# Optimization experiments

Hardware: AMD Instinct MI355X
Metric: run time of the kernel (lower is better)

The kernel has to match this reference:

```python
import jax, jax.numpy as jnp
import numpy as np

LATENT = 128
K = 1024          # num_embeddings
LENGTH = 128
HID = 200         # LSTM hidden
IN = 768
COND = 1536


def setup_inputs() -> dict:
    key = jax.random.key(0)
    ks = jax.random.split(key, 16)
    B = 256
    x = jax.random.normal(ks[0], (B, 1, LENGTH, IN), dtype=jnp.float32)
    condition = jax.random.normal(ks[1], (B, 1, LENGTH, COND), dtype=jnp.float32)
    noise = jax.random.normal(ks[2], (B, IN), dtype=jnp.float32)
    s = 0.05
    # LSTM params (PyTorch gate order: i, f, g, o)
    W_ih = jax.random.normal(ks[3], (4 * HID, IN), dtype=jnp.float32) * s
    W_hh = jax.random.normal(ks[4], (4 * HID, HID), dtype=jnp.float32) * s
    b_ih = jax.random.normal(ks[5], (4 * HID,), dtype=jnp.float32) * s
    b_hh = jax.random.normal(ks[6], (4 * HID,), dtype=jnp.float32) * s
    # encoder fc: HID -> LATENT
    W_enc = jax.random.normal(ks[7], (LATENT, HID), dtype=jnp.float32) * s
    b_enc = jnp.zeros((LATENT,), dtype=jnp.float32)
    # codebook, uniform(-1/K, 1/K) as in the module
    emb = jax.random.uniform(ks[8], (K, LATENT), minval=-1.0 / K, maxval=1.0 / K, dtype=jnp.float32)
    # decoder MLP
    D1_IN = LATENT + COND + IN  # 2432
    W1 = jax.random.normal(ks[9], (200, D1_IN), dtype=jnp.float32) * s
    b1 = jnp.zeros((200,), dtype=jnp.float32)
    W2 = jax.random.normal(ks[10], (400, 200), dtype=jnp.float32) * s
    b2 = jnp.zeros((400,), dtype=jnp.float32)
    W3 = jax.random.normal(ks[11], (IN, 400), dtype=jnp.float32) * s
    b3 = jnp.zeros((IN,), dtype=jnp.float32)
    return {"x": x, "condition": condition, "noise": noise,
            "W_ih": W_ih, "W_hh": W_hh, "b_ih": b_ih, "b_hh": b_hh,
            "W_enc": W_enc, "b_enc": b_enc, "emb": emb,
            "W1": W1, "b1": b1, "W2": W2, "b2": b2, "W3": W3, "b3": b3}


def _lstm_last_h(xs, W_ih, W_hh, b_ih, b_hh):
    # xs: [B, T, IN] -> final hidden state [B, HID]
    B = xs.shape[0]
    h0 = jnp.zeros((B, HID), dtype=xs.dtype)
    c0 = jnp.zeros((B, HID), dtype=xs.dtype)
    # precompute input projections for all timesteps: [T, B, 4H]
    gates_x = jnp.einsum('bti,gi->tbg', xs, W_ih) + b_ih + b_hh

    def step(carry, gx):
        h, c = carry
        g = gx + h @ W_hh.T  # [B, 4H]
        i, f, gg, o = jnp.split(g, 4, axis=-1)
        c = jax.nn.sigmoid(f) * c + jax.nn.sigmoid(i) * jnp.tanh(gg)
        h = jax.nn.sigmoid(o) * jnp.tanh(c)
        return (h, c), None

    (h, _), _ = jax.lax.scan(step, (h0, c0), gates_x)
    return h


def reference(x, condition, noise, W_ih, W_hh, b_ih, b_hh, W_enc, b_enc, emb,
              W1, b1, W2, b2, W3, b3):
    B = x.shape[0]
    # Encoder
    xs = x.reshape(B, -1, IN)                      # [B, T, 768]
    h = _lstm_last_h(xs, W_ih, W_hh, b_ih, b_hh)   # [B, 200]
    z_e = h @ W_enc.T + b_enc                      # [B, latent]
    # VectorQuantizer: squared-distance argmin + gather
    d = (jnp.sum(z_e * z_e, axis=-1, keepdims=True)
         + jnp.sum(emb * emb, axis=1)
         - 2.0 * z_e @ emb.T)                      # [B, K]
    indices = jnp.argmin(d, axis=-1)               # [B]
    z_q = emb[indices]                             # [B, latent]
    # Decoder (forward uses z_q directly)
    L = LENGTH
    z = jnp.broadcast_to(z_q[:, None, None, :], (B, 1, L, LATENT))
    n = jnp.broadcast_to(noise[:, None, None, :], (B, 1, L, IN))
    zc = jnp.concatenate([z, condition, n], axis=-1)  # [B,1,L,2432]
    h1 = jax.nn.relu(zc @ W1.T + b1)
    h2 = jax.nn.relu(h1 @ W2.T + b2)
    out = jax.nn.sigmoid(h2 @ W3.T + b3)
    return out.reshape(-1, 1, L, IN)
```

## Files before the change

### kernel.cpp

```cpp
#include <hip/hip_runtime.h>
#include <math.h>

typedef unsigned short u16;
typedef u16 u16x8 __attribute__((ext_vector_type(8)));
typedef __bf16 bf16x8 __attribute__((ext_vector_type(8)));
typedef float f32x4 __attribute__((ext_vector_type(4)));

#define HID 200
#define G4H 800
#define TLEN 128
#define LATENT 128
#define NCODES 1024
#define DIN 768
#define DCOND 1536
#define NB 256
#define MROWS (NB * TLEN)
#define LDG 896
#define LDH1 256
#define LDH2 512
#define NOUT 768

#define WSCL 400.0f
#define HSCL 127.0f
#define ISCL (1.0f / (WSCL * HSCL))
#define W4_UINT4 (12 * 800)
#define W4_BYTES (W4_UINT4 * 16)

__device__ __forceinline__ u16 f2b(float f) {
  union { float f; unsigned u; } v; v.f = f;
  unsigned r = v.u + 0x7fffu + ((v.u >> 16) & 1u);
  return (u16)(r >> 16);
}
__device__ __forceinline__ float b2f(u16 h) {
  union { unsigned u; float f; } v; v.u = ((unsigned)h) << 16;
  return v.f;
}
__device__ __forceinline__ float sigf(float x) { return 1.f / (1.f + __expf(-x)); }
__device__ __forceinline__ float tanh_fast(float x) {
  return 1.f - 2.f / (__expf(2.f * x) + 1.f);
}

__device__ __forceinline__ int dot4(unsigned a, unsigned b, int c) {
#if __has_builtin(__builtin_amdgcn_sdot4)
  return __builtin_amdgcn_sdot4((int)a, (int)b, c, false);
#else
  int s = c;
  s += (int)(signed char)(a) * (int)(signed char)(b);
  s += (int)(signed char)(a >> 8) * (int)(signed char)(b >> 8);
  s += (int)(signed char)(a >> 16) * (int)(signed char)(b >> 16);
  s += (int)(signed char)(a >> 24) * (int)(signed char)(b >> 24);
  return s;
#endif
}

__device__ __forceinline__ void gl16(const void* g, void* l) {
  __builtin_amdgcn_global_load_lds(
      (const __attribute__((address_space(1))) void*)g,
      (__attribute__((address_space(3))) void*)l, 16, 0, 0);
}

__device__ __forceinline__ unsigned cvtpk(float a, float b) {
  unsigned r;
  asm("v_cvt_pk_bf16_f32 %0, %1, %2" : "=v"(r) : "v"(a), "v"(b));
  return r;
}

__global__ void cvt_pad(const float* __restrict__ src, u16* __restrict__ dst,
                        int nr, int nc, int lds, int col0, int NRp, int KP) {
  int i = blockIdx.x * blockDim.x + threadIdx.x;
  if (i >= NRp * KP) return;
  int r = i / KP, c = i - r * KP;
  float v = (r < nr && c < nc) ? src[(size_t)r * lds + col0 + c] : 0.f;
  dst[i] = f2b(v);
}

__global__ void pad_f32(const float* __restrict__ src, float* __restrict__ dst,
                        int n, int npad) {
  int i = blockIdx.x * blockDim.x + threadIdx.x;
  if (i < npad) dst[i] = (i < n) ? src[i] : 0.f;
}

__global__ void pack_whh_i8(const float* __restrict__ Whh, unsigned* __restrict__ W4,
                            unsigned* __restrict__ Wreg,
                            const float* __restrict__ b_ih, const float* __restrict__ b_hh,
                            float* __restrict__ biasc) {
  int i = blockIdx.x * blockDim.x + threadIdx.x;
  if (i < 800 * 50) {
    int row = i / 50, dw = i - row * 50;
    unsigned d = 0;
#pragma unroll
    for (int e = 0; e < 4; ++e) {
      int k = dw * 4 + e;
      float w = Whh[(size_t)row * HID + k] * WSCL;
      int q = (int)lrintf(w);
      q = q > 127 ? 127 : (q < -127 ? -127 : q);
      d |= ((unsigned)(q & 0xFF)) << (8 * e);
    }
    if (dw < 48) {
      W4[((dw >> 2) * 800 + row) * 4 + (dw & 3)] = d;
    } else {
      int g = row / 200, u = row - g * 200;
      Wreg[u * 8 + g * 2 + (dw - 48)] = d;
    }
  }
  if (i < LDG) biasc[i] = (i < G4H) ? (b_ih[i] + b_hh[i]) : 0.f;
}

enum { EPI_GATES = 0, EPI_H1 = 1, EPI_H2 = 2, EPI_OUT = 3 };

__device__ __forceinline__ f32x4 mfma16(bf16x8 a, bf16x8 b, f32x4 c) {
  return __builtin_amdgcn_mfma_f32_16x16x32_bf16(a, b, c, 0, 0, 0);
}

template<bool AF32, int EPI>
__global__ __launch_bounds__(256) void gemm_bf16(
    const void* __restrict__ Ap, const u16* __restrict__ Bp,
    void* __restrict__ Cp, int K, int ldc, const float* __restrict__ bias) {
  __shared__ __attribute__((aligned(16))) char AsRaw[AF32 ? 128 * 32 * 4 : 128 * 32 * 2];
  __shared__ __attribute__((aligned(16))) u16 Bs[128 * 32];
  float* Asf = (float*)AsRaw;
  u16* As16 = (u16*)AsRaw;

  const int t = threadIdx.x;
  const int tileN = blockIdx.x * 128;
  const int tileM = blockIdx.y * 128;
  const int l = t & 63;
  const int w = t >> 6;
  const int wr = (w >> 1) * 64;
  const int wc = (w & 1) * 64;
  const int fr = l & 15;
  const int fg = l >> 4;

  const u16* bsrc[2];
  u16* bdst[2];
#pragma unroll
  for (int j = 0; j < 2; ++j) {
    int tb = w * 1024 + j * 4096 + (t & 63) * 16;
    int row = tb >> 6, gd = (tb >> 4) & 3;
    bsrc[j] = Bp + (size_t)(tileN + row) * K + ((gd ^ ((row >> 1) & 3)) << 3);
    bdst[j] = Bs + w * 512 + j * 2048;
  }
  const float* asrcF[4];
  float* adstF[4];
  const u16* asrcH[2];
  u16* adstH[2];
  if constexpr (AF32) {
#pragma unroll
    for (int j = 0; j < 4; ++j) {
      int tb = w * 1024 + j * 4096 + (t & 63) * 16;
      int row = tb >> 7, gd = (tb >> 4) & 7;
      asrcF[j] = (const float*)Ap + (size_t)(tileM + row) * K + ((gd ^ (row & 7)) << 2);
      adstF[j] = Asf + w * 256 + j * 1024;
    }
  } else {
#pragma unroll
    for (int j = 0; j < 2; ++j) {
      int tb = w * 1024 + j * 4096 + (t & 63) * 16;
      int row = tb >> 6, gd = (tb >> 4) & 3;
      asrcH[j] = (const u16*)Ap + (size_t)(tileM + row) * K + ((gd ^ ((row >> 1) & 3)) << 3);
      adstH[j] = As16 + w * 512 + j * 2048;
    }
  }

  f32x4 acc[4][4];
#pragma unroll
  for (int m = 0; m < 4; ++m)
#pragma unroll
    for (int n = 0; n < 4; ++n) {
      f32x4 z = {0.f, 0.f, 0.f, 0.f};
      acc[m][n] = z;
    }

  for (int k0 = 0; k0 < K; k0 += 32) {
#pragma unroll
    for (int j = 0; j < 2; ++j) { gl16(bsrc[j], bdst[j]); bsrc[j] += 32; }
    if constexpr (AF32) {
#pragma unroll
      for (int j = 0; j < 4; ++j) { gl16(asrcF[j], adstF[j]); asrcF[j] += 32; }
    } else {
#pragma unroll
      for (int j = 0; j < 2; ++j) { gl16(asrcH[j], adstH[j]); asrcH[j] += 32; }
    }
    __syncthreads();

    bf16x8 av[4], bv[4];
#pragma unroll
    for (int m = 0; m < 4; ++m) {
      const int row = wr + m * 16 + fr;
      if constexpr (AF32) {
        const int g0 = (2 * fg) ^ (row & 7);
        const int g1 = (2 * fg + 1) ^ (row & 7);
        float4 p0 = *(const float4*)(Asf + row * 32 + g0 * 4);
        float4 p1 = *(const float4*)(Asf + row * 32 + g1 * 4);
        uint4 u;
        u.x = cvtpk(p0.x, p0.y); u.y = cvtpk(p0.z, p0.w);
        u.z = cvtpk(p1.x, p1.y); u.w = cvtpk(p1.z, p1.w);
        av[m] = __builtin_bit_cast(bf16x8, u);
      } else {
        const int g = fg ^ ((row >> 1) & 3);
        av[m] = __builtin_bit_cast(bf16x8, *(const u16x8*)(As16 + row * 32 + g * 8));
      }
    }
#pragma unroll
    for (int n = 0; n < 4; ++n) {
      const int row = wc + n * 16 + fr;
      const int g = fg ^ ((row >> 1) & 3);
      bv[n] = __builtin_bit_cast(bf16x8, *(const u16x8*)(Bs + row * 32 + g * 8));
    }
#pragma unroll
    for (int m = 0; m < 4; ++m)
#pragma unroll
      for (int n = 0; n < 4; ++n)
        acc[m][n] = mfma16(av[m], bv[n], acc[m][n]);
    __syncthreads();
  }

#pragma unroll
  for (int m = 0; m < 4; ++m) {
#pragma unroll
    for (int n = 0; n < 4; ++n) {
      const int gcol = tileN + wc + n * 16 + fr;
      const int growb = tileM + wr + m * 16 + fg * 4;
#pragma unroll
      for (int r = 0; r < 4; ++r) {
        const int grow = growb + r;
        float v = acc[m][n][r];
        if constexpr (EPI == EPI_GATES) {
          v += bias[gcol];
          ((u16*)Cp)[(size_t)grow * ldc + gcol] = f2b(v);
        } else if constexpr (EPI == EPI_H1) {
          v += bias[(grow >> 7) * 256 + gcol];
          v = fmaxf(v, 0.f);
          ((u16*)Cp)[(size_t)grow * ldc + gcol] = f2b(v);
        } else if constexpr (EPI == EPI_H2) {
          v += bias[gcol];
          v = fmaxf(v, 0.f);
          ((u16*)Cp)[(size_t)grow * ldc + gcol] = f2b(v);
        } else {
          v += bias[gcol];
          ((float*)Cp)[(size_t)grow * ldc + gcol] = sigf(v);
        }
      }
    }
  }
}

__global__ __launch_bounds__(256) void lstm_enc(
    const u16* __restrict__ gates, const uint4* __restrict__ W4g,
    const uint4* __restrict__ WregG,
    const float* __restrict__ Wenc, const float* __restrict__ b_enc,
    const float* __restrict__ emb, const float* __restrict__ W1,
    const float* __restrict__ b1, const float* __restrict__ noise,
    float* __restrict__ p1) {
  extern __shared__ __attribute__((aligned(16))) char dynsm[];
  uint4* W4 = (uint4*)dynsm;
  __shared__ __attribute__((aligned(16))) unsigned sh_hq[2][56];
  __shared__ __attribute__((aligned(16))) float sh_hf[HID];
  __shared__ __attribute__((aligned(16))) float sh_ze[LATENT];
  __shared__ float sh_zq[LATENT];
  __shared__ float sh_rd[256];
  __shared__ int sh_ri[256];
  const int r = threadIdx.x;
  const int b = blockIdx.x;
  const bool worker = (r < 200);

  for (int i = r; i < W4_UINT4; i += 256) W4[i] = W4g[i];
  uint4 wt0 = {0, 0, 0, 0}, wt1 = {0, 0, 0, 0};
  if (worker) { wt0 = WregG[r * 2]; wt1 = WregG[r * 2 + 1]; }
  if (r < 56) { sh_hq[0][r] = 0; sh_hq[1][r] = 0; }
  float c = 0.f, hlast = 0.f;
  const u16* gp = gates + (size_t)b * TLEN * LDG + r;
  float gv0 = 0.f, gv1 = 0.f, gv2 = 0.f, gv3 = 0.f;
  if (worker) {
    gv0 = b2f(gp[0]); gv1 = b2f(gp[200]);
    gv2 = b2f(gp[400]); gv3 = b2f(gp[600]);
  }
  __syncthreads();

  for (int t = 0; t < TLEN; ++t) {
    gp += LDG;
    float gn0 = 0.f, gn1 = 0.f, gn2 = 0.f, gn3 = 0.f;
    if (worker && t + 1 < TLEN) {
      gn0 = b2f(gp[0]); gn1 = b2f(gp[200]);
      gn2 = b2f(gp[400]); gn3 = b2f(gp[600]);
    }
    const int cur = t & 1, nxt = cur ^ 1;

    if (worker) {
      unsigned hd[52];
#pragma unroll
      for (int j = 0; j < 13; ++j) {
        uint4 v = ((const uint4*)sh_hq[cur])[j];
        hd[4 * j + 0] = v.x; hd[4 * j + 1] = v.y;
        hd[4 * j + 2] = v.z; hd[4 * j + 3] = v.w;
      }
      int a0 = 0, a1 = 0, a2 = 0, a3 = 0;
#pragma unroll
      for (int jb = 0; jb < 12; ++jb) {
        uint4 w0 = W4[jb * 800 + r];
        uint4 w1 = W4[jb * 800 + 200 + r];
        uint4 w2 = W4[jb * 800 + 400 + r];
        uint4 w3 = W4[jb * 800 + 600 + r];
#pragma unroll
        for (int e = 0; e < 4; ++e) {
          unsigned h = hd[jb * 4 + e];
          a0 = dot4((&w0.x)[e], h, a0);
          a1 = dot4((&w1.x)[e], h, a1);
          a2 = dot4((&w2.x)[e], h, a2);
          a3 = dot4((&w3.x)[e], h, a3);
        }
      }
      a0 = dot4(wt0.x, hd[48], a0); a0 = dot4(wt0.y, hd[49], a0);
      a1 = dot4(wt0.z, hd[48], a1); a1 = dot4(wt0.w, hd[49], a1);
      a2 = dot4(wt1.x, hd[48], a2); a2 = dot4(wt1.y, hd[49], a2);
      a3 = dot4(wt1.z, hd[48], a3); a3 = dot4(wt1.w, hd[49], a3);
      float gi = gv0 + (float)a0 * ISCL;
      float gf = gv1 + (float)a1 * ISCL;
      float gg = gv2 + (float)a2 * ISCL;
      float go = gv3 + (float)a3 * ISCL;
      c = sigf(gf) * c + sigf(gi) * tanh_fast(gg);
      hlast = sigf(go) * tanh_fast(c);
      ((char*)sh_hq[nxt])[r] = (char)__float2int_rn(hlast * HSCL);
    }
    __syncthreads();
    gv0 = gn0; gv1 = gn1; gv2 = gn2; gv3 = gn3;
  }

  if (worker) sh_hf[r] = hlast;
  __syncthreads();

  if (r < LATENT) {
    float z = b_enc[r];
#pragma unroll 4
    for (int k = 0; k < HID; ++k) z = fmaf(Wenc[(size_t)r * HID + k], sh_hf[k], z);
    sh_ze[r] = z;
  }
  __syncthreads();

  float best = INFINITY; int bi = 0;
  for (int k = r; k < NCODES; k += 256) {
    float d = 0.f;
#pragma unroll
    for (int q = 0; q < LATENT / 4; ++q) {
      float4 e = *(const float4*)&emb[(size_t)k * LATENT + q * 4];
      float4 z = *(const float4*)&sh_ze[q * 4];
      d += e.x * (e.x - 2.f * z.x) + e.y * (e.y - 2.f * z.y)
         + e.z * (e.z - 2.f * z.z) + e.w * (e.w - 2.f * z.w);
    }
    if (d < best) { best = d; bi = k; }
  }
  sh_rd[r] = best; sh_ri[r] = bi;
  __syncthreads();
  for (int s = 128; s > 0; s >>= 1) {
    if (r < s) {
      float od = sh_rd[r + s]; int oi = sh_ri[r + s];
      if (od < sh_rd[r] || (od == sh_rd[r] && oi < sh_ri[r])) { sh_rd[r] = od; sh_ri[r] = oi; }
    }
    __syncthreads();
  }
  const int kmin = sh_ri[0];
  if (r < LATENT) sh_zq[r] = emb[(size_t)kmin * LATENT + r];
  __syncthreads();

  {
    float v = 0.f;
    if (worker) {
      v = b1[r];
      const float* wrow = W1 + (size_t)r * 2432;
#pragma unroll 4
      for (int d = 0; d < LATENT; ++d) v = fmaf(wrow[d], sh_zq[d], v);
      const float* nz = noise + (size_t)b * DIN;
#pragma unroll 4
      for (int d = 0; d < DIN; ++d) v = fmaf(wrow[1664 + d], nz[d], v);
    }
    p1[b * 256 + r] = v;
  }
}

extern "C" void kernel_launch(void* const* d_in, const int* in_sizes, int n_in,
                              void* d_out, int out_size, void* d_ws, size_t ws_size,
                              hipStream_t stream) {
  const float* x     = (const float*)d_in[0];
  const float* cond  = (const float*)d_in[1];
  const float* noise = (const float*)d_in[2];
  const float* W_ih  = (const float*)d_in[3];
  const float* W_hh  = (const float*)d_in[4];
  const float* b_ih  = (const float*)d_in[5];
  const float* b_hh  = (const float*)d_in[6];
  const float* W_enc = (const float*)d_in[7];
  const float* b_enc = (const float*)d_in[8];
  const float* emb   = (const float*)d_in[9];
  const float* W1    = (const float*)d_in[10];
  const float* b1    = (const float*)d_in[11];
  const float* W2    = (const float*)d_in[12];
  const float* b2    = (const float*)d_in[13];
  const float* W3    = (const float*)d_in[14];
  const float* b3    = (const float*)d_in[15];

  char* ws = (char*)d_ws;
  size_t off = 0;
  auto alloc = [&](size_t bytes) -> void* {
    void* p = ws + off; off += (bytes + 255) & ~(size_t)255; return p;
  };
  u16*      W_ihb = (u16*)alloc((size_t)896 * 768 * 2);
  u16*      W1cb  = (u16*)alloc((size_t)256 * 1536 * 2);
  u16*      W2b   = (u16*)alloc((size_t)512 * 256 * 2);
  u16*      W3b   = (u16*)alloc((size_t)768 * 512 * 2);
  float*    b2p   = (float*)alloc(512 * 4);
  unsigned* W4    = (unsigned*)alloc((size_t)W4_BYTES);
  unsigned* Wreg  = (unsigned*)alloc((size_t)200 * 8 * 4);
  float*    biasc = (float*)alloc(LDG * 4);
  u16*      gates = (u16*)alloc((size_t)MROWS * LDG * 2);
  float*    p1    = (float*)alloc(256 * 256 * 4);
  u16*      h1    = (u16*)alloc((size_t)MROWS * LDH1 * 2);
  u16*      h2    = (u16*)alloc((size_t)MROWS * LDH2 * 2);

  cvt_pad<<<dim3((896 * 768 + 255) / 256), 256, 0, stream>>>(W_ih, W_ihb, 800, 768, 768, 0, 896, 768);
  cvt_pad<<<dim3((256 * 1536 + 255) / 256), 256, 0, stream>>>(W1, W1cb, 200, 1536, 2432, 128, 256, 1536);
  cvt_pad<<<dim3((512 * 256 + 255) / 256), 256, 0, stream>>>(W2, W2b, 400, 200, 200, 0, 512, 256);
  cvt_pad<<<dim3((768 * 512 + 255) / 256), 256, 0, stream>>>(W3, W3b, 768, 400, 400, 0, 768, 512);
  pad_f32<<<dim3(2), 256, 0, stream>>>(b2, b2p, 400, 512);
  pack_whh_i8<<<dim3((800 * 50 + 255) / 256), 256, 0, stream>>>(W_hh, W4, Wreg, b_ih, b_hh, biasc);

  gemm_bf16<true, EPI_GATES><<<dim3(LDG / 128, MROWS / 128), 256, 0, stream>>>(
      x, W_ihb, gates, 768, LDG, biasc);

  static bool attr_set = false;
  if (!attr_set) {
    (void)hipFuncSetAttribute((const void*)lstm_enc,
                              hipFuncAttributeMaxDynamicSharedMemorySize, W4_BYTES);
    attr_set = true;
  }
  lstm_enc<<<dim3(NB), 256, W4_BYTES, stream>>>(gates, (const uint4*)W4, (const uint4*)Wreg,
                                                W_enc, b_enc, emb, W1, b1, noise, p1);

  gemm_bf16<true, EPI_H1><<<dim3(LDH1 / 128, MROWS / 128), 256, 0, stream>>>(
      cond, W1cb, h1, DCOND, LDH1, p1);
  gemm_bf16<false, EPI_H2><<<dim3(LDH2 / 128, MROWS / 128), 256, 0, stream>>>(
      h1, W2b, h2, LDH1, LDH2, b2p);
  gemm_bf16<false, EPI_OUT><<<dim3(NOUT / 128, MROWS / 128), 256, 0, stream>>>(
      h2, W3b, (float*)d_out, LDH2, NOUT, b3);
}
```

Measured before the change: 555.4 us.

## Split LSTM recurrent dot products across two thread halves per hidden unit

The LSTM block grows from 256 to 512 threads. Each of the 200 hidden units now has two threads: one computes the int8 dot products over the first half of the hidden vector, the other over the second half, and partial sums are combined through shared memory. This halves the serial per-thread work on the 128-step recurrent critical path. The cost is an extra __syncthreads per timestep plus shared-memory traffic, and fewer concurrent blocks per CU because of higher thread counts and register pressure.

```diff
diff --git a/kernel.cpp b/kernel.cpp
--- a/kernel.cpp
+++ b/kernel.cpp
@@ -245,7 +245,7 @@
   }
 }
 
-__global__ __launch_bounds__(256) void lstm_enc(
+__global__ __launch_bounds__(512) void lstm_enc(
     const u16* __restrict__ gates, const uint4* __restrict__ W4g,
     const uint4* __restrict__ WregG,
     const float* __restrict__ Wenc, const float* __restrict__ b_enc,
@@ -255,23 +255,27 @@
   extern __shared__ __attribute__((aligned(16))) char dynsm[];
   uint4* W4 = (uint4*)dynsm;
   __shared__ __attribute__((aligned(16))) unsigned sh_hq[2][56];
+  __shared__ __attribute__((aligned(16))) int sh_p[4][208];
   __shared__ __attribute__((aligned(16))) float sh_hf[HID];
   __shared__ __attribute__((aligned(16))) float sh_ze[LATENT];
   __shared__ float sh_zq[LATENT];
-  __shared__ float sh_rd[256];
-  __shared__ int sh_ri[256];
+  __shared__ float sh_rd[512];
+  __shared__ int sh_ri[512];
   const int r = threadIdx.x;
   const int b = blockIdx.x;
-  const bool worker = (r < 200);
-
-  for (int i = r; i < W4_UINT4; i += 256) W4[i] = W4g[i];
+  const bool act = (r < 400);
+  const int u = (r < 200) ? r : r - 200;
+  const bool lo = (r < 200);
+  const bool hi = act && !lo;
+
+  for (int i = r; i < W4_UINT4; i += 512) W4[i] = W4g[i];
   uint4 wt0 = {0, 0, 0, 0}, wt1 = {0, 0, 0, 0};
-  if (worker) { wt0 = WregG[r * 2]; wt1 = WregG[r * 2 + 1]; }
+  if (lo) { wt0 = WregG[u * 2]; wt1 = WregG[u * 2 + 1]; }
   if (r < 56) { sh_hq[0][r] = 0; sh_hq[1][r] = 0; }
   float c = 0.f, hlast = 0.f;
-  const u16* gp = gates + (size_t)b * TLEN * LDG + r;
+  const u16* gp = gates + (size_t)b * TLEN * LDG + u;
   float gv0 = 0.f, gv1 = 0.f, gv2 = 0.f, gv3 = 0.f;
-  if (worker) {
+  if (lo) {
     gv0 = b2f(gp[0]); gv1 = b2f(gp[200]);
     gv2 = b2f(gp[400]); gv3 = b2f(gp[600]);
   }
@@ -280,53 +284,65 @@
   for (int t = 0; t < TLEN; ++t) {
     gp += LDG;
     float gn0 = 0.f, gn1 = 0.f, gn2 = 0.f, gn3 = 0.f;
-    if (worker && t + 1 < TLEN) {
+    if (lo && t + 1 < TLEN) {
       gn0 = b2f(gp[0]); gn1 = b2f(gp[200]);
       gn2 = b2f(gp[400]); gn3 = b2f(gp[600]);
     }
     const int cur = t & 1, nxt = cur ^ 1;
 
-    if (worker) {
-      unsigned hd[52];
-#pragma unroll
-      for (int j = 0; j < 13; ++j) {
-        uint4 v = ((const uint4*)sh_hq[cur])[j];
+    int a0 = 0, a1 = 0, a2 = 0, a3 = 0;
+    if (act) {
+      const int jb0 = lo ? 0 : 6;
+      unsigned hd[24];
+#pragma unroll
+      for (int j = 0; j < 6; ++j) {
+        uint4 v = ((const uint4*)sh_hq[cur])[(lo ? 0 : 6) + j];
         hd[4 * j + 0] = v.x; hd[4 * j + 1] = v.y;
         hd[4 * j + 2] = v.z; hd[4 * j + 3] = v.w;
       }
-      int a0 = 0, a1 = 0, a2 = 0, a3 = 0;
-#pragma unroll
-      for (int jb = 0; jb < 12; ++jb) {
-        uint4 w0 = W4[jb * 800 + r];
-        uint4 w1 = W4[jb * 800 + 200 + r];
-        uint4 w2 = W4[jb * 800 + 400 + r];
-        uint4 w3 = W4[jb * 800 + 600 + r];
+#pragma unroll
+      for (int j = 0; j < 6; ++j) {
+        const int jb = jb0 + j;
+        uint4 w0 = W4[jb * 800 + u];
+        uint4 w1 = W4[jb * 800 + 200 + u];
+        uint4 w2 = W4[jb * 800 + 400 + u];
+        uint4 w3 = W4[jb * 800 + 600 + u];
 #pragma unroll
         for (int e = 0; e < 4; ++e) {
-          unsigned h = hd[jb * 4 + e];
+          unsigned h = hd[j * 4 + e];
           a0 = dot4((&w0.x)[e], h, a0);
           a1 = dot4((&w1.x)[e], h, a1);
           a2 = dot4((&w2.x)[e], h, a2);
           a3 = dot4((&w3.x)[e], h, a3);
         }
       }
-      a0 = dot4(wt0.x, hd[48], a0); a0 = dot4(wt0.y, hd[49], a0);
-      a1 = dot4(wt0.z, hd[48], a1); a1 = dot4(wt0.w, hd[49], a1);
-      a2 = dot4(wt1.x, hd[48], a2); a2 = dot4(wt1.y, hd[49], a2);
-      a3 = dot4(wt1.z, hd[48], a3); a3 = dot4(wt1.w, hd[49], a3);
-      float gi = gv0 + (float)a0 * ISCL;
-      float gf = gv1 + (float)a1 * ISCL;
-      float gg = gv2 + (float)a2 * ISCL;
-      float go = gv3 + (float)a3 * ISCL;
+      if (hi) {
+        sh_p[0][u] = a0; sh_p[1][u] = a1;
+        sh_p[2][u] = a2; sh_p[3][u] = a3;
+      }
+    }
+    if (lo) {
+      uint2 ht = *(const uint2*)&sh_hq[cur][48];
+      a0 = dot4(wt0.x, ht.x, a0); a0 = dot4(wt0.y, ht.y, a0);
+      a1 = dot4(wt0.z, ht.x, a1); a1 = dot4(wt0.w, ht.y, a1);
+      a2 = dot4(wt1.x, ht.x, a2); a2 = dot4(wt1.y, ht.y, a2);
+      a3 = dot4(wt1.z, ht.x, a3); a3 = dot4(wt1.w, ht.y, a3);
+    }
+    __syncthreads();
+    if (lo) {
+      float gi = gv0 + (float)(a0 + sh_p[0][u]) * ISCL;
+      float gf = gv1 + (float)(a1 + sh_p[1][u]) * ISCL;
+      float gg = gv2 + (float)(a2 + sh_p[2][u]) * ISCL;
+      float go = gv3 + (float)(a3 + sh_p[3][u]) * ISCL;
       c = sigf(gf) * c + sigf(gi) * tanh_fast(gg);
       hlast = sigf(go) * tanh_fast(c);
-      ((char*)sh_hq[nxt])[r] = (char)__float2int_rn(hlast * HSCL);
+      ((char*)sh_hq[nxt])[u] = (char)__float2int_rn(hlast * HSCL);
     }
     __syncthreads();
     gv0 = gn0; gv1 = gn1; gv2 = gn2; gv3 = gn3;
   }
 
-  if (worker) sh_hf[r] = hlast;
+  if (lo) sh_hf[u] = hlast;
   __syncthreads();
 
   if (r < LATENT) {
@@ -338,7 +354,7 @@
   __syncthreads();
 
   float best = INFINITY; int bi = 0;
-  for (int k = r; k < NCODES; k += 256) {
+  for (int k = r; k < NCODES; k += 512) {
     float d = 0.f;
 #pragma unroll
     for (int q = 0; q < LATENT / 4; ++q) {
@@ -351,7 +367,7 @@
   }
   sh_rd[r] = best; sh_ri[r] = bi;
   __syncthreads();
-  for (int s = 128; s > 0; s >>= 1) {
+  for (int s = 256; s > 0; s >>= 1) {
     if (r < s) {
       float od = sh_rd[r + s]; int oi = sh_ri[r + s];
       if (od < sh_rd[r] || (od == sh_rd[r] && oi < sh_ri[r])) { sh_rd[r] = od; sh_ri[r] = oi; }
@@ -362,9 +378,9 @@
   if (r < LATENT) sh_zq[r] = emb[(size_t)kmin * LATENT + r];
   __syncthreads();
 
-  {
+  if (r < 256) {
     float v = 0.f;
-    if (worker) {
+    if (r < HID) {
       v = b1[r];
       const float* wrow = W1 + (size_t)r * 2432;
 #pragma unroll 4
@@ -431,7 +447,7 @@
                               hipFuncAttributeMaxDynamicSharedMemorySize, W4_BYTES);
     attr_set = true;
   }
-  lstm_enc<<<dim3(NB), 256, W4_BYTES, stream>>>(gates, (const uint4*)W4, (const uint4*)Wreg,
+  lstm_enc<<<dim3(NB), 512, W4_BYTES, stream>>>(gates, (const uint4*)W4, (const uint4*)Wreg,
                                                 W_enc, b_enc, emb, W1, b1, noise, p1);
 
   gemm_bf16<true, EPI_H1><<<dim3(LDH1 / 128, MROWS / 128), 256, 0, stream>>>(
```

Result: faster. 524.4 us (-5.6%).
